# Kernel tuning notes

Measured on AMD Instinct MI355X. Metric: run time of the kernel, lower is better.

## Reference

```python
import jax, jax.numpy as jnp
import numpy as np

# truncation bit counts per layer (from Net __init__ kwargs); relu uses n=0 (no-op)
N_CONV1 = 13
N_CONV2 = 13
N_FC1 = 13
N_FC2 = 13
HIDDEN = 500
BATCH = 4096


def trunc(x, n):
    """Zero out the low n bits of the float32 mantissa (bitwise, like numpy round-trip in torch code)."""
    if n == 0:
        return x
    b = jax.lax.bitcast_convert_type(x, jnp.int32) & np.int32(-1 << n)
    return jax.lax.bitcast_convert_type(b, jnp.float32)


def conv2d(x, w, b):
    # NCHW / OIHW, stride 1, VALID padding (padding=0 in torch module)
    y = jax.lax.conv_general_dilated(x, w, window_strides=(1, 1), padding='VALID',
                                     dimension_numbers=('NCHW', 'OIHW', 'NCHW'))
    return y + b[None, :, None, None]


def max_pool_2x2(x):
    return jax.lax.reduce_window(x, -jnp.inf, jax.lax.max,
                                 window_dimensions=(1, 1, 2, 2),
                                 window_strides=(1, 1, 2, 2), padding='VALID')


def setup_inputs() -> dict:
    key = jax.random.key(0)
    ks = jax.random.split(key, 9)
    x = jax.random.normal(ks[0], (BATCH, 1, 28, 28), dtype=jnp.float32)
    # kaiming-uniform-ish init scales (fan_in based)
    def u(k, shape, fan_in):
        bound = 1.0 / np.sqrt(fan_in)
        return jax.random.uniform(k, shape, jnp.float32, -bound, bound)
    w_conv1 = u(ks[1], (20, 1, 5, 5), 1 * 25)
    b_conv1 = u(ks[2], (20,), 1 * 25)
    w_conv2 = u(ks[3], (50, 20, 5, 5), 20 * 25)
    b_conv2 = u(ks[4], (50,), 20 * 25)
    w_fc1 = u(ks[5], (HIDDEN, 800), 800)
    b_fc1 = u(ks[6], (HIDDEN,), 800)
    w_fc2 = u(ks[7], (10, HIDDEN), HIDDEN)
    b_fc2 = u(ks[8], (10,), HIDDEN)
    return {"x": x, "w_conv1": w_conv1, "b_conv1": b_conv1,
            "w_conv2": w_conv2, "b_conv2": b_conv2,
            "w_fc1": w_fc1, "b_fc1": b_fc1,
            "w_fc2": w_fc2, "b_fc2": b_fc2}


def reference(x, w_conv1, b_conv1, w_conv2, b_conv2, w_fc1, b_fc1, w_fc2, b_fc2):
    # conv1 -> trunc -> relu (relu n=0, so plain relu)
    h = jnp.maximum(trunc(conv2d(x, w_conv1, b_conv1), N_CONV1), 0.0)   # [B,20,24,24]
    h = max_pool_2x2(h)                                                  # [B,20,12,12]
    h = jnp.maximum(trunc(conv2d(h, w_conv2, b_conv2), N_CONV2), 0.0)   # [B,50,8,8]
    h = max_pool_2x2(h)                                                  # [B,50,4,4]
    h = h.reshape(-1, 4 * 4 * 50)                                        # [B,800]
    h = jnp.maximum(trunc(h @ w_fc1.T + b_fc1[None, :], N_FC1), 0.0)    # [B,HIDDEN]
    h = trunc(h @ w_fc2.T + b_fc2[None, :], N_FC2)                       # [B,10]
    return jax.nn.log_softmax(h, axis=1)
```

## Files before the change

kernel.cpp:

```cpp
#include <hip/hip_runtime.h>


typedef _Float16 v8h __attribute__((ext_vector_type(8)));
typedef float v4f __attribute__((ext_vector_type(4)));

__device__ __forceinline__ float trunc13(float v) {
    return __int_as_float(__float_as_int(v) & (int)0xFFFFE000u);
}

__global__ void k_prep(const float* __restrict__ w1, const float* __restrict__ w2,
                       const float* __restrict__ wf1,
                       _Float16* __restrict__ wpc1, _Float16* __restrict__ wph,
                       _Float16* __restrict__ wpf1) {
    int id = blockIdx.x * 256 + threadIdx.x;
    if (id < 1280) {
        int t = id >> 6, oc = id & 63;
        _Float16* dh = wph + (size_t)id * 32;
        for (int s = 0; s < 32; ++s) {
            int k = t * 32 + s;
            int pix = (k * 2731) >> 16;
            int icr = k - pix * 24;
            float w = 0.f;
            if (pix < 25 && icr < 20 && oc < 50)
                w = w2[oc * 500 + icr * 25 + pix];
            dh[s] = (_Float16)w;
        }
    } else if (id < 1408) {
        int l = id - 1280;
        int lane = l & 63, tile = l >> 6;
        int rr = lane & 15, kg = lane >> 4;
        int oc = tile * 16 + rr;
        _Float16* dst = wpc1 + (size_t)l * 8;
        for (int j = 0; j < 8; ++j) {
            int t = kg * 8 + j;
            float w = (oc < 20 && t < 25) ? w1[oc * 25 + t] : 0.f;
            dst[j] = (_Float16)w;
        }
    } else if (id < 14208) {
        int id2 = id - 1408;
        int t = id2 >> 9, oc = id2 & 511;
        _Float16* dst = wpf1 + (size_t)id2 * 64;
        for (int kk = 0; kk < 32; ++kk) {
            float w = (oc < 500) ? wf1[(size_t)oc * 800 + t * 32 + kk] : 0.f;
            _Float16 hi = (_Float16)w;
            dst[kk] = hi;
            dst[32 + kk] = (_Float16)(w - (float)hi);
        }
    }
}

__global__ __launch_bounds__(256) void k_conv1(const float* __restrict__ x,
                                               const _Float16* __restrict__ wpc1,
                                               const float* __restrict__ b1,
                                               _Float16* __restrict__ p1h) {
    int tid = threadIdx.x;
    int wid = tid >> 6, lane = tid & 63;
    int b = blockIdx.x * 4 + wid;
    int kg = lane >> 4, rr = lane & 15;
    int py = rr >> 2, px = rr & 3;

    v8h bf0 = *(const v8h*)(wpc1 + (size_t)lane * 8);
    v8h bf1 = *(const v8h*)(wpc1 + (size_t)(64 + lane) * 8);
    float bias0 = b1[rr];
    float bias1 = (rr < 4) ? b1[16 + rr] : 0.f;

    int off[8];
#pragma unroll
    for (int j = 0; j < 8; ++j) {
        int t = kg * 8 + j;
        if (t > 24) t = 24;
        int ky = (t * 205) >> 10;
        int kx = t - 5 * ky;
        off[j] = (py + ky) * 28 + (px + kx);
    }

    const float* img = x + (size_t)b * 784;
    _Float16* outb = p1h + (size_t)b * 144 * 24;

    for (int qy = 0; qy < 6; ++qy) {
#pragma unroll
        for (int qx = 0; qx < 6; ++qx) {
            const float* base = img + (qy * 4) * 28 + qx * 4;
            v8h a;
#pragma unroll
            for (int j = 0; j < 8; ++j) a[j] = (_Float16)base[off[j]];

            v4f acc0 = {0.f, 0.f, 0.f, 0.f}, acc1 = {0.f, 0.f, 0.f, 0.f};
            acc0 = __builtin_amdgcn_mfma_f32_16x16x32_f16(a, bf0, acc0, 0, 0, 0);
            acc1 = __builtin_amdgcn_mfma_f32_16x16x32_f16(a, bf1, acc1, 0, 0, 0);

            float z0 = fmaxf(trunc13(acc0[0] + bias0), 0.f);
            float z1 = fmaxf(trunc13(acc0[1] + bias0), 0.f);
            float z2 = fmaxf(trunc13(acc0[2] + bias0), 0.f);
            float z3 = fmaxf(trunc13(acc0[3] + bias0), 0.f);
            float m01 = fmaxf(z0, z1), m23 = fmaxf(z2, z3);
            float p01 = fmaxf(m01, __shfl_xor(m01, 16, 64));
            float p23 = fmaxf(m23, __shfl_xor(m23, 16, 64));
            float y0 = fmaxf(trunc13(acc1[0] + bias1), 0.f);
            float y1 = fmaxf(trunc13(acc1[1] + bias1), 0.f);
            float y2 = fmaxf(trunc13(acc1[2] + bias1), 0.f);
            float y3 = fmaxf(trunc13(acc1[3] + bias1), 0.f);
            float n01 = fmaxf(y0, y1), n23 = fmaxf(y2, y3);
            float q01 = fmaxf(n01, __shfl_xor(n01, 16, 64));
            float q23 = fmaxf(n23, __shfl_xor(n23, 16, 64));

            if (!(kg & 1)) {
                int pos0 = (2 * qy + (kg >> 1)) * 12 + 2 * qx;
                _Float16* o = outb + (size_t)pos0 * 24;
                o[rr]      = (_Float16)p01;
                o[24 + rr] = (_Float16)p23;
                if (rr < 4) {
                    o[16 + rr]      = (_Float16)q01;
                    o[24 + 16 + rr] = (_Float16)q23;
                }
            }
        }
    }
}

#define AIMG3 3744
__global__ __launch_bounds__(256, 2) void k_conv2(const _Float16* __restrict__ p1h,
                                                  const _Float16* __restrict__ wph,
                                                  const float* __restrict__ b2,
                                                  _Float16* __restrict__ p2h) {
    __shared__ __align__(16) _Float16 Al[8 * AIMG3];
    int tid = threadIdx.x;
    int b0 = blockIdx.x * 8;

    {
        const uint4* src = (const uint4*)(p1h + (size_t)b0 * 3456);
        uint4* dst = (uint4*)Al;
        uint4 z = make_uint4(0u, 0u, 0u, 0u);
        for (int i = tid; i < 3744; i += 256) {
            int img = i / 468, r = i - img * 468;
            dst[i] = (r < 432) ? src[img * 432 + r] : z;
        }
    }
    __syncthreads();

    int wid = tid >> 6, lane = tid & 63;
    int kg = lane >> 4, rr = lane & 15;
    int Y = rr >> 3, xx = rr & 7;
    const _Float16* Ab0 = Al + (wid * 2) * AIMG3;
    const _Float16* Ab1 = Ab0 + AIMG3;
    const _Float16* abase[8];
#pragma unroll
    for (int my = 0; my < 4; ++my) {
        abase[my]     = Ab0 + ((2 * my + Y) * 12 + xx) * 24;
        abase[my + 4] = Ab1 + ((2 * my + Y) * 12 + xx) * 24;
    }
    const _Float16* bh_base = wph + rr * 32 + kg * 8;

    v4f acc[8][4];
#pragma unroll
    for (int my = 0; my < 8; ++my)
#pragma unroll
        for (int nt = 0; nt < 4; ++nt) acc[my][nt] = (v4f){0.f, 0.f, 0.f, 0.f};

#define CSTEP(T, BV)                                                          \
    {                                                                         \
        int k0 = (T) * 32 + kg * 8;                                           \
        int pix = (k0 * 2731) >> 16;                                          \
        int icol = k0 - pix * 24;                                             \
        int ky = (pix * 205) >> 10;                                           \
        int kx = pix - 5 * ky;                                                \
        int aofs = (ky * 12 + kx) * 24 + icol;                                \
        v8h af[8];                                                            \
        _Pragma("unroll")                                                     \
        for (int my = 0; my < 8; ++my)                                        \
            af[my] = *(const v8h*)(abase[my] + aofs);                         \
        _Pragma("unroll")                                                     \
        for (int my = 0; my < 8; ++my)                                        \
            _Pragma("unroll")                                                 \
            for (int nt = 0; nt < 4; ++nt)                                    \
                acc[my][nt] = __builtin_amdgcn_mfma_f32_16x16x32_f16(         \
                    af[my], BV[nt], acc[my][nt], 0, 0, 0);                    \
    }

    for (int u = 0; u < 9; ++u) {
        int t0 = 2 * u, t1 = 2 * u + 1;
        v8h bA[4], bB[4];
#pragma unroll
        for (int nt = 0; nt < 4; ++nt) {
            bA[nt] = *(const v8h*)(bh_base + t0 * 2048 + nt * 512);
            bB[nt] = *(const v8h*)(bh_base + t1 * 2048 + nt * 512);
        }
        CSTEP(t0, bA);
        CSTEP(t1, bB);
    }
    {
        v8h bA[4];
#pragma unroll
        for (int nt = 0; nt < 4; ++nt)
            bA[nt] = *(const v8h*)(bh_base + 18 * 2048 + nt * 512);
        CSTEP(18, bA);
    }
#undef CSTEP

#pragma unroll
    for (int h = 0; h < 2; ++h) {
        int imgg = b0 + wid * 2 + h;
#pragma unroll
        for (int nt = 0; nt < 4; ++nt) {
            int oc = nt * 16 + rr;
            float bias = (oc < 50) ? b2[oc] : 0.f;
#pragma unroll
            for (int my = 0; my < 4; ++my) {
                v4f a = acc[h * 4 + my][nt];
                float z0 = fmaxf(trunc13(a[0] + bias), 0.f);
                float z1 = fmaxf(trunc13(a[1] + bias), 0.f);
                float z2 = fmaxf(trunc13(a[2] + bias), 0.f);
                float z3 = fmaxf(trunc13(a[3] + bias), 0.f);
                float s0 = fmaxf(z0, z1), s2 = fmaxf(z2, z3);
                float o0 = fmaxf(s0, __shfl_xor(s0, 32, 64));
                float o2 = fmaxf(s2, __shfl_xor(s2, 32, 64));
                if (kg < 2 && oc < 50) {
                    p2h[(size_t)imgg * 800 + oc * 16 + my * 4 + 2 * kg]     = (_Float16)o0;
                    p2h[(size_t)imgg * 800 + oc * 16 + my * 4 + 2 * kg + 1] = (_Float16)o2;
                }
            }
        }
    }
}

__global__ __launch_bounds__(256) void k_fc1(const _Float16* __restrict__ Ah,
                                             const _Float16* __restrict__ Bp,
                                             const float* __restrict__ bias,
                                             _Float16* __restrict__ Hh) {
    int tid = threadIdx.x;
    int i0 = blockIdx.x * 128, n0 = blockIdx.y * 64;
    int wid = tid >> 6, lane = tid & 63;
    int rr = lane & 15, kg = lane >> 4;

    const _Float16* arow[2];
#pragma unroll
    for (int mf = 0; mf < 2; ++mf)
        arow[mf] = Ah + (size_t)(i0 + wid * 32 + mf * 16 + rr) * 800 + kg * 8;
    const _Float16* brow[4];
#pragma unroll
    for (int nf = 0; nf < 4; ++nf)
        brow[nf] = Bp + (size_t)(n0 + nf * 16 + rr) * 64 + kg * 8;

    v4f acc[2][4];
#pragma unroll
    for (int mf = 0; mf < 2; ++mf)
#pragma unroll
        for (int nf = 0; nf < 4; ++nf) acc[mf][nf] = (v4f){0.f, 0.f, 0.f, 0.f};

    for (int t = 0; t < 25; ++t) {
        v8h af[2], bh[4];
#pragma unroll
        for (int mf = 0; mf < 2; ++mf)
            af[mf] = *(const v8h*)(arow[mf] + t * 32);
#pragma unroll
        for (int nf = 0; nf < 4; ++nf)
            bh[nf] = *(const v8h*)(brow[nf] + (size_t)t * 32768);
#pragma unroll
        for (int mf = 0; mf < 2; ++mf)
#pragma unroll
            for (int nf = 0; nf < 4; ++nf)
                acc[mf][nf] = __builtin_amdgcn_mfma_f32_16x16x32_f16(af[mf], bh[nf], acc[mf][nf], 0, 0, 0);
    }

#pragma unroll
    for (int mf = 0; mf < 2; ++mf)
#pragma unroll
        for (int nf = 0; nf < 4; ++nf) {
            int col = n0 + nf * 16 + rr;
            float bs = bias[col < 500 ? col : 0];
#pragma unroll
            for (int j = 0; j < 4; ++j) {
                int row = i0 + wid * 32 + mf * 16 + kg * 4 + j;
                float v = fmaxf(trunc13(acc[mf][nf][j] + bs), 0.f);
                if (col < 500) Hh[(size_t)row * 512 + col] = (_Float16)v;
            }
        }
}

__global__ __launch_bounds__(256) void k_fc2(const _Float16* __restrict__ Hh,
                                             const float* __restrict__ W,
                                             const float* __restrict__ bias,
                                             float* __restrict__ out) {
    int wave = threadIdx.x >> 6;
    int lane = threadIdx.x & 63;
    int i = blockIdx.x * 4 + wave;
    const _Float16* hrow = Hh + (size_t)i * 512;

    float p[10];
#pragma unroll
    for (int j = 0; j < 10; ++j) p[j] = 0.f;
    for (int k = lane; k < 500; k += 64) {
        float h = (float)hrow[k];
#pragma unroll
        for (int j = 0; j < 10; ++j) p[j] += h * W[j * 500 + k];
    }
#pragma unroll
    for (int j = 0; j < 10; ++j)
#pragma unroll
        for (int off = 32; off; off >>= 1) p[j] += __shfl_xor(p[j], off, 64);

    if (lane == 0) {
        float z[10], m = -1e30f;
#pragma unroll
        for (int j = 0; j < 10; ++j) {
            z[j] = trunc13(p[j] + bias[j]);
            m = fmaxf(m, z[j]);
        }
        float s = 0.f;
#pragma unroll
        for (int j = 0; j < 10; ++j) s += expf(z[j] - m);
        float lse = m + logf(s);
#pragma unroll
        for (int j = 0; j < 10; ++j) out[(size_t)i * 10 + j] = z[j] - lse;
    }
}

extern "C" void kernel_launch(void* const* d_in, const int* in_sizes, int n_in,
                              void* d_out, int out_size, void* d_ws, size_t ws_size,
                              hipStream_t stream) {
    const float* x   = (const float*)d_in[0];
    const float* w1  = (const float*)d_in[1];
    const float* b1  = (const float*)d_in[2];
    const float* w2  = (const float*)d_in[3];
    const float* b2  = (const float*)d_in[4];
    const float* wf1 = (const float*)d_in[5];
    const float* bf1 = (const float*)d_in[6];
    const float* wf2 = (const float*)d_in[7];
    const float* bf2 = (const float*)d_in[8];
    float* out = (float*)d_out;

    char* ws = (char*)d_ws;
    _Float16* p1h  = (_Float16*)(ws);
    _Float16* p2h  = (_Float16*)(ws + 28311552);
    _Float16* h1h  = (_Float16*)(ws + 34865152);
    _Float16* wph  = (_Float16*)(ws + 39059456);
    _Float16* wpf1 = (_Float16*)(ws + 39141376);
    _Float16* wpc1 = (_Float16*)(ws + 40779776);

    k_prep<<<56, 256, 0, stream>>>(w1, w2, wf1, wpc1, wph, wpf1);
    k_conv1<<<1024, 256, 0, stream>>>(x, wpc1, b1, p1h);
    k_conv2<<<512, 256, 0, stream>>>(p1h, wph, b2, p2h);
    dim3 g3(32, 8);
    k_fc1<<<g3, 256, 0, stream>>>(p2h, wpf1, bf1, h1h);
    k_fc2<<<1024, 256, 0, stream>>>(h1h, wf2, bf2, out);
}
```

Before: 100.5 us.

## Double-buffer fc1 operands through LDS and raise wave priority around conv MFMAs

The fc1 GEMM now stages A and B tiles into swizzled, double-buffered shared memory, prefetching the next K-slice from global into registers while MFMAs run on the current one. Before this, each wave loaded its fragments straight from global memory, so the same data was fetched redundantly across waves. Separately, the conv2 MFMA block is wrapped in s_setprio to favour waves issuing matrix work. The costs are extra LDS traffic and a barrier on every iteration of the fc1 loop.

```diff
diff --git a/kernel.cpp b/kernel.cpp
--- a/kernel.cpp
+++ b/kernel.cpp
@@ -169,12 +169,14 @@
         _Pragma("unroll")                                                     \
         for (int my = 0; my < 8; ++my)                                        \
             af[my] = *(const v8h*)(abase[my] + aofs);                         \
+        __builtin_amdgcn_s_setprio(1);                                        \
         _Pragma("unroll")                                                     \
         for (int my = 0; my < 8; ++my)                                        \
             _Pragma("unroll")                                                 \
             for (int nt = 0; nt < 4; ++nt)                                    \
                 acc[my][nt] = __builtin_amdgcn_mfma_f32_16x16x32_f16(         \
                     af[my], BV[nt], acc[my][nt], 0, 0, 0);                    \
+        __builtin_amdgcn_s_setprio(0);                                        \
     }
 
     for (int u = 0; u < 9; ++u) {
@@ -227,39 +229,68 @@
                                              const _Float16* __restrict__ Bp,
                                              const float* __restrict__ bias,
                                              _Float16* __restrict__ Hh) {
+    __shared__ _Float16 Al[2][4096];
+    __shared__ _Float16 Bl[2][2560];
     int tid = threadIdx.x;
     int i0 = blockIdx.x * 128, n0 = blockIdx.y * 64;
     int wid = tid >> 6, lane = tid & 63;
     int rr = lane & 15, kg = lane >> 4;
 
-    const _Float16* arow[2];
+    int ca0 = tid, ca1 = tid + 256;
+    int ra0_ = ca0 >> 2, qa0 = ca0 & 3, ra1_ = ca1 >> 2, qa1 = ca1 & 3;
+    int aw0 = (ra0_ * 4 + (qa0 ^ ((ra0_ >> 1) & 3))) * 8;
+    int aw1 = (ra1_ * 4 + (qa1 ^ ((ra1_ >> 1) & 3))) * 8;
+    int bwB = ((tid >> 2) * 5 + (tid & 3)) * 8;
+
+    uint4 xa0, xa1, xb0;
+    auto loadT = [&](int t) {
+        xa0 = *(const uint4*)(Ah + (size_t)(i0 + ra0_) * 800 + t * 32 + qa0 * 8);
+        xa1 = *(const uint4*)(Ah + (size_t)(i0 + ra1_) * 800 + t * 32 + qa1 * 8);
+        const uint4* g = (const uint4*)Bp + (size_t)t * 4096 + (size_t)n0 * 8;
+        xb0 = g[(tid >> 2) * 8 + (tid & 3)];
+    };
+    auto writeT = [&](int buf) {
+        *(uint4*)(&Al[buf][aw0]) = xa0;
+        *(uint4*)(&Al[buf][aw1]) = xa1;
+        *(uint4*)(&Bl[buf][bwB]) = xb0;
+    };
+
+    int aoff[2], bhoff[4];
+#pragma unroll
+    for (int mf = 0; mf < 2; ++mf) {
+        int r = wid * 32 + mf * 16 + rr;
+        aoff[mf] = (r * 4 + (kg ^ ((rr >> 1) & 3))) * 8;
+    }
+#pragma unroll
+    for (int nf = 0; nf < 4; ++nf)
+        bhoff[nf] = ((nf * 16 + rr) * 5 + kg) * 8;
+
+    v4f zero = {0.f, 0.f, 0.f, 0.f};
+    v4f acc[2][4];
 #pragma unroll
     for (int mf = 0; mf < 2; ++mf)
-        arow[mf] = Ah + (size_t)(i0 + wid * 32 + mf * 16 + rr) * 800 + kg * 8;
-    const _Float16* brow[4];
-#pragma unroll
-    for (int nf = 0; nf < 4; ++nf)
-        brow[nf] = Bp + (size_t)(n0 + nf * 16 + rr) * 64 + kg * 8;
-
-    v4f acc[2][4];
-#pragma unroll
-    for (int mf = 0; mf < 2; ++mf)
-#pragma unroll
-        for (int nf = 0; nf < 4; ++nf) acc[mf][nf] = (v4f){0.f, 0.f, 0.f, 0.f};
+#pragma unroll
+        for (int nf = 0; nf < 4; ++nf) acc[mf][nf] = zero;
+
+    loadT(0);
+    writeT(0);
+    __syncthreads();
 
     for (int t = 0; t < 25; ++t) {
+        int cur = t & 1;
+        if (t < 24) loadT(t + 1);
         v8h af[2], bh[4];
 #pragma unroll
-        for (int mf = 0; mf < 2; ++mf)
-            af[mf] = *(const v8h*)(arow[mf] + t * 32);
-#pragma unroll
-        for (int nf = 0; nf < 4; ++nf)
-            bh[nf] = *(const v8h*)(brow[nf] + (size_t)t * 32768);
+        for (int mf = 0; mf < 2; ++mf) af[mf] = *(const v8h*)(&Al[cur][aoff[mf]]);
+#pragma unroll
+        for (int nf = 0; nf < 4; ++nf) bh[nf] = *(const v8h*)(&Bl[cur][bhoff[nf]]);
 #pragma unroll
         for (int mf = 0; mf < 2; ++mf)
 #pragma unroll
             for (int nf = 0; nf < 4; ++nf)
                 acc[mf][nf] = __builtin_amdgcn_mfma_f32_16x16x32_f16(af[mf], bh[nf], acc[mf][nf], 0, 0, 0);
+        if (t < 24) writeT(cur ^ 1);
+        __syncthreads();
     }
 
 #pragma unroll
```

Measured after the change: 96.61 us. 1.04x faster.
